# Kernel optimization log

Hardware: AMD Instinct MI355X
Metric: run time of the kernel (lower is better)

Reference implementation:

```python
import jax, jax.numpy as jnp
import numpy as np

B, N, E = 4, 25000, 1600000
NODE_DIM, EMBED = 64, 64
NUM = B * N


def setup_inputs() -> dict:
    key = jax.random.key(0)
    ks = jax.random.split(key, 12)
    p = lambda k, s: jax.random.normal(k, s, jnp.float32) * 0.05
    z = lambda s: jnp.zeros(s, jnp.float32)
    return {
        "node_feat": jax.random.normal(ks[0], (B, N, NODE_DIM), jnp.float32),
        "src": jax.random.randint(ks[1], (E,), 0, NUM),
        "dst": jax.random.randint(ks[2], (E,), 0, NUM),
        "edge_weight": jax.random.uniform(ks[3], (E,), jnp.float32),
        "h": z((NUM, EMBED)),
        "W_cz": p(ks[4], (NODE_DIM, EMBED)), "b_cz": z((EMBED,)),
        "W_cr": p(ks[5], (NODE_DIM, EMBED)), "b_cr": z((EMBED,)),
        "W_ch": p(ks[6], (NODE_DIM, EMBED)), "b_ch": z((EMBED,)),
        "W_lz": p(ks[7], (2 * EMBED, EMBED)), "b_lz": z((EMBED,)),
        "W_lr": p(ks[8], (2 * EMBED, EMBED)), "b_lr": z((EMBED,)),
        "W_lh": p(ks[9], (2 * EMBED, EMBED)), "b_lh": z((EMBED,)),
        "W_head": p(ks[10], (EMBED, 1)), "b_head": z((1,)),
    }


def gcn_conv(x, W, b, src, dst, ew):
    # PyG GCNConv: self-loops (fill=1) + symmetric normalization, then linear.
    n = x.shape[0]
    loop = jnp.arange(n)
    s = jnp.concatenate([src, loop])
    d = jnp.concatenate([dst, loop])
    w = jnp.concatenate([ew, jnp.ones((n,), x.dtype)])
    deg = jax.ops.segment_sum(w, d, num_segments=n)
    dinv = jnp.where(deg > 0, jax.lax.rsqrt(deg), 0.0)
    norm = dinv[s] * w * dinv[d]                      # [E+n]
    xw = x @ W                                        # [n, EMBED]
    out = jax.ops.segment_sum(xw[s] * norm[:, None], d, num_segments=n)
    return out + b


def tgcn_cell(x, h, src, dst, ew,
              W_cz, b_cz, W_cr, b_cr, W_ch, b_ch,
              W_lz, b_lz, W_lr, b_lr, W_lh, b_lh):
    Z = jax.nn.sigmoid(
        jnp.concatenate([gcn_conv(x, W_cz, b_cz, src, dst, ew), h], axis=1) @ W_lz + b_lz)
    R = jax.nn.sigmoid(
        jnp.concatenate([gcn_conv(x, W_cr, b_cr, src, dst, ew), h], axis=1) @ W_lr + b_lr)
    H_tilde = jnp.tanh(
        jnp.concatenate([gcn_conv(x, W_ch, b_ch, src, dst, ew), h * R], axis=1) @ W_lh + b_lh)
    return Z * h + (1.0 - Z) * H_tilde


def reference(node_feat, src, dst, edge_weight, h,
              W_cz, b_cz, W_cr, b_cr, W_ch, b_ch,
              W_lz, b_lz, W_lr, b_lr, W_lh, b_lh,
              W_head, b_head):
    Bv, Nv, _ = node_feat.shape
    x = node_feat.reshape(Bv * Nv, -1)
    h0 = tgcn_cell(x, h, src, dst, edge_weight,
                   W_cz, b_cz, W_cr, b_cr, W_ch, b_ch,
                   W_lz, b_lz, W_lr, b_lr, W_lh, b_lh)
    z = jax.nn.relu(h0)
    z = (z @ W_head + b_head).reshape(Bv, Nv, -1)
    return (z, h0)
```

## Files before the change

### kernel.cpp

```cpp
#include <hip/hip_runtime.h>
#include <hip/hip_fp16.h>
#include <stdint.h>

typedef unsigned long long u64;
typedef _Float16 half8 __attribute__((ext_vector_type(8)));
typedef float f32x4 __attribute__((ext_vector_type(4)));

#define EPB 6144
#define CAPC 5440

__device__ __forceinline__ float sigm(float x) { return 1.0f / (1.0f + __expf(-x)); }
__device__ __forceinline__ float tanhfast(float x) { return 1.0f - 2.0f / (__expf(2.0f * x) + 1.0f); }
__device__ __forceinline__ int rli(int v, int k) { return __builtin_amdgcn_readlane(v, k); }
__device__ __forceinline__ float rlf(float v, int k) {
    return __int_as_float(__builtin_amdgcn_readlane(__float_as_int(v), k));
}

__global__ void k_pre(const float* __restrict__ Wcz, const float* __restrict__ bcz,
                      const float* __restrict__ Wcr, const float* __restrict__ bcr,
                      const float* __restrict__ Wch, const float* __restrict__ bch,
                      const float* __restrict__ Wlz, const float* __restrict__ blz,
                      const float* __restrict__ Wlr, const float* __restrict__ blr,
                      const float* __restrict__ Wlh, const float* __restrict__ blh,
                      const float4* __restrict__ h4, __half* __restrict__ aggh,
                      __half* __restrict__ B1f, __half* __restrict__ B2f,
                      float* __restrict__ bias, int* __restrict__ cursor, int hq) {
    int bid = blockIdx.x;
    if (bid < 113) {
        int tid = bid * 256 + threadIdx.x;
        if (tid < 1024) cursor[tid] = 0;
        if (tid < 24576) {
            int k = tid / 192, nc = tid % 192;
            int g = nc >> 6, j = nc & 63;
            const float* Wc = (g == 0) ? Wcz : (g == 1) ? Wcr : Wch;
            const float* Wl = (g == 0) ? Wlz : (g == 1) ? Wlr : Wlh;
            float v;
            if (k < 64) {
                float acc = 0.f;
                for (int m = 0; m < 64; m++) acc += Wc[k * 64 + m] * Wl[m * 64 + j];
                v = acc;
            } else {
                v = (g < 2) ? Wl[k * 64 + j] : 0.f;
            }
            int kt = k >> 5, nt = nc >> 4;
            int lane = (((k >> 3) & 3) << 4) | (nc & 15);
            B1f[(((kt * 12 + nt) * 64 + lane) << 3) + (k & 7)] = (__half)v;
        } else if (tid < 24576 + 4096) {
            int t = tid - 24576;
            int k = t >> 6, nc = t & 63;
            float v = Wlh[(64 + k) * 64 + nc];
            int kt = k >> 5, nt = nc >> 4;
            int lane = (((k >> 3) & 3) << 4) | (nc & 15);
            B2f[(((kt * 4 + nt) * 64 + lane) << 3) + (k & 7)] = (__half)v;
        } else if (tid < 24576 + 4096 + 192) {
            int t = tid - 24576 - 4096;
            int g = t >> 6, j = t & 63;
            const float* bc = (g == 0) ? bcz : (g == 1) ? bcr : bch;
            const float* Wl = (g == 0) ? Wlz : (g == 1) ? Wlr : Wlh;
            const float* bl = (g == 0) ? blz : (g == 1) ? blr : blh;
            float acc = bl[j];
            for (int m = 0; m < 64; m++) acc += bc[m] * Wl[m * 64 + j];
            bias[t] = acc;
        }
    } else {
        int i = (bid - 113) * 256 + threadIdx.x;
        if (i < hq) {
            float4 hv = h4[i];
            int elem = i * 4;
            int node = elem >> 6, c = elem & 63;
            __half2* ho = (__half2*)(aggh + (((size_t)node) << 7) + 64 + c);
            ho[0] = __floats2half2_rn(hv.x, hv.y);
            ho[1] = __floats2half2_rn(hv.z, hv.w);
        }
    }
}

__global__ void __launch_bounds__(1024) k_bin(const int* __restrict__ src, const int* __restrict__ dst,
                                              const float* __restrict__ ew,
                                              int* __restrict__ cursor, u64* __restrict__ binned,
                                              int E, int R) {
    __shared__ u64 recs[EPB];
    __shared__ int hist[512];
    __shared__ int loff[512];
    __shared__ int curL[512];
    __shared__ int gbase[512];

    int tid = threadIdx.x;
    if (tid < 512) hist[tid] = 0;
    __syncthreads();

    int base = blockIdx.x * EPB;
    int cntE = min(EPB, E - base);

    u64 myrec[6];
    int myr[6];
#pragma unroll
    for (int j = 0; j < 6; j++) {
        int idx = tid + j * 1024;
        if (idx < cntE) {
            int e = base + idx;
            int d = dst[e], s = src[e];
            float w = ew[e];
            int r = d >> 8;
            myr[j] = r;
            myrec[j] = (u64)((unsigned)s | ((unsigned)(d & 255) << 17)) | ((u64)__float_as_uint(w) << 32);
            atomicAdd(&hist[r], 1);
        } else myr[j] = -1;
    }
    __syncthreads();

    if (tid < 64) {
        int sums[8], tot = 0;
#pragma unroll
        for (int q = 0; q < 8; q++) { sums[q] = hist[tid * 8 + q]; tot += sums[q]; }
        int scan = tot;
#pragma unroll
        for (int o = 1; o < 64; o <<= 1) {
            int v = __shfl_up(scan, o);
            if (tid >= o) scan += v;
        }
        int run = scan - tot;
#pragma unroll
        for (int q = 0; q < 8; q++) { loff[tid * 8 + q] = run; run += sums[q]; }
    }
    if (tid < 512) curL[tid] = 0;
    if (tid < R) {
        int hcnt = hist[tid];
        if (hcnt > 0) gbase[tid] = tid * CAPC + atomicAdd(&cursor[tid], hcnt);
    }
    __syncthreads();

#pragma unroll
    for (int j = 0; j < 6; j++) {
        if (myr[j] >= 0) {
            int p = atomicAdd(&curL[myr[j]], 1);
            recs[loff[myr[j]] + p] = myrec[j];
        }
    }
    __syncthreads();

    int wave = tid >> 6, lane = tid & 63;
    for (int r = wave; r < R; r += 16) {
        int len = hist[r];
        if (!len) continue;
        int gb = gbase[r], lo = loff[r];
        int capEnd = (r + 1) * CAPC;
        for (int i = lane; i < len; i += 64)
            if (gb + i < capEnd) binned[(size_t)(gb + i)] = recs[lo + i];
    }
}

__global__ void __launch_bounds__(1024) k_sort(const int* __restrict__ cursor,
                                               u64* __restrict__ binned,
                                               const float2* __restrict__ x2,
                                               float* __restrict__ dinv,
                                               __half2* __restrict__ xs2,
                                               int* __restrict__ off_g, int* __restrict__ len_g,
                                               int n) {
    __shared__ u64 srt[CAPC];
    __shared__ int hist[256];
    __shared__ int noff[256];
    __shared__ int cur[256];
    __shared__ float degw[256];

    int r = blockIdx.x, tid = threadIdx.x;
    if (tid < 256) { hist[tid] = 0; degw[tid] = 0.f; }
    __syncthreads();

    int cnt = min(cursor[r], CAPC);
    u64* B = binned + (size_t)r * CAPC;

    for (int i = tid; i < cnt; i += 1024) {
        u64 m = B[i];
        int dl = ((unsigned)m >> 17) & 255;
        atomicAdd(&hist[dl], 1);
        atomicAdd(&degw[dl], __uint_as_float((unsigned)(m >> 32)));
    }
    __syncthreads();

    if (tid < 64) {
        int s0 = hist[tid * 4], s1 = hist[tid * 4 + 1], s2 = hist[tid * 4 + 2], s3 = hist[tid * 4 + 3];
        int tot = s0 + s1 + s2 + s3;
        int scan = tot;
#pragma unroll
        for (int o = 1; o < 64; o <<= 1) {
            int v = __shfl_up(scan, o);
            if (tid >= o) scan += v;
        }
        int run = scan - tot;
        noff[tid * 4] = run; run += s0;
        noff[tid * 4 + 1] = run; run += s1;
        noff[tid * 4 + 2] = run; run += s2;
        noff[tid * 4 + 3] = run;
    }
    __syncthreads();

    if (tid < 256) {
        int node = r * 256 + tid;
        float dv = rsqrtf(1.0f + degw[tid]);
        if (node < n) {
            dinv[node] = dv;
            off_g[node] = r * CAPC + noff[tid];
            len_g[node] = hist[tid];
        }
        cur[tid] = noff[tid];
        degw[tid] = dv;
    }
    __syncthreads();

    for (int i = tid; i < cnt; i += 1024) {
        u64 m = B[i];
        int dl = ((unsigned)m >> 17) & 255;
        int p = atomicAdd(&cur[dl], 1);
        srt[p] = (u64)((unsigned)m & 0x1FFFF) | (m & 0xFFFFFFFF00000000ULL);
    }
    __syncthreads();

    for (int i = tid; i < cnt; i += 1024) B[i] = srt[i];
    int nbase = r * 256;
    for (int i = tid; i < 256 * 32; i += 1024) {
        int nl = i >> 5, cp = i & 31;
        int node = nbase + nl;
        if (node < n) {
            float2 xv = x2[((size_t)node << 5) + cp];
            float dv = degw[nl];
            xs2[((size_t)node << 5) + cp] = __floats2half2_rn(dv * xv.x, dv * xv.y);
        }
    }
}

__global__ void __launch_bounds__(256) k_gather(const int* __restrict__ off_g, const int* __restrict__ len_g,
                                                const u64* __restrict__ csr, const float* __restrict__ dinv,
                                                const __half* __restrict__ xs,
                                                __half* __restrict__ aggh, int n) {
    int lane = threadIdx.x & 63;
    int wid = __builtin_amdgcn_readfirstlane((int)(threadIdx.x >> 6));
    int d = blockIdx.x * 4 + wid;
    if (d >= n) return;
    int o0 = off_g[d], L = len_g[d];
    float dd = dinv[d];

    const uint2* __restrict__ rp = (const uint2*)(csr + (size_t)o0);

    float acc[8];
#pragma unroll
    for (int j = 0; j < 8; j++) acc[j] = 0.f;
    acc[0] = (float)xs[((size_t)d << 6) + lane];

    int k = 0;
    for (; k + 8 <= L; k += 8) {
        uint2 r[8];
#pragma unroll
        for (int j = 0; j < 8; j++) r[j] = rp[k + j];
#pragma unroll
        for (int j = 0; j < 8; j++) {
            acc[j] = fmaf(__uint_as_float(r[j].y),
                          (float)xs[((size_t)r[j].x << 6) + lane], acc[j]);
        }
    }
    for (; k < L; k++) {
        uint2 r = rp[k];
        acc[0] = fmaf(__uint_as_float(r.y),
                      (float)xs[((size_t)r.x << 6) + lane], acc[0]);
    }

    float s = ((acc[0] + acc[1]) + (acc[2] + acc[3])) + ((acc[4] + acc[5]) + (acc[6] + acc[7]));
    aggh[((size_t)d << 7) + lane] = (__half)(dd * s);
}

__global__ void __launch_bounds__(256, 2) k_node(
        const __half* __restrict__ aggh,
        const __half* __restrict__ B1f_g, const __half* __restrict__ B2f_g,
        const float* __restrict__ bias_g, const float* __restrict__ Whead,
        const float* __restrict__ bhead,
        float* __restrict__ out_head, float* __restrict__ out_h, int n) {

    __shared__ __half B1s[24576];
    __shared__ __half B2s[4096];
    __shared__ float biasS[192];
    __shared__ float whS[64];
    __shared__ __half hrb[4][16 * 72];

    int tid = threadIdx.x;
    {
        const uint4* s1 = (const uint4*)B1f_g; uint4* d1 = (uint4*)B1s;
        for (int i = tid; i < 3072; i += 256) d1[i] = s1[i];
        const uint4* s2 = (const uint4*)B2f_g; uint4* d2 = (uint4*)B2s;
        for (int i = tid; i < 512; i += 256) d2[i] = s2[i];
        if (tid < 192) biasS[tid] = bias_g[tid];
        if (tid < 64) whS[tid] = Whead[tid];
    }
    __syncthreads();

    int lane = tid & 63;
    int wave = tid >> 6;
    int quad = lane >> 4;
    int l15 = lane & 15;

    float bz4[4], br4[4], bh4[4], wh4[4];
#pragma unroll
    for (int nt = 0; nt < 4; nt++) {
        bz4[nt] = biasS[nt * 16 + l15];
        br4[nt] = biasS[64 + nt * 16 + l15];
        bh4[nt] = biasS[128 + nt * 16 + l15];
        wh4[nt] = whS[nt * 16 + l15];
    }
    float bhv = bhead[0];
    __half* myhr = &hrb[wave][0];
    const half8* B1v = (const half8*)B1s;
    const half8* B2v = (const half8*)B2s;

    int mbase = blockIdx.x * 64 + wave * 16;
    if (mbase < n) {
        const half8* arow = (const half8*)(aggh + (((size_t)(mbase + l15)) << 7) + (quad << 3));
        half8 a0 = arow[0], a1 = arow[4], a2 = arow[8], a3 = arow[12];

        f32x4 acc[12];
#pragma unroll
        for (int nt = 0; nt < 12; nt++) acc[nt] = (f32x4){0.f, 0.f, 0.f, 0.f};

#pragma unroll
        for (int nt = 0; nt < 12; nt++) {
            acc[nt] = __builtin_amdgcn_mfma_f32_16x16x32_f16(a0, B1v[(0 * 12 + nt) * 64 + lane], acc[nt], 0, 0, 0);
            acc[nt] = __builtin_amdgcn_mfma_f32_16x16x32_f16(a1, B1v[(1 * 12 + nt) * 64 + lane], acc[nt], 0, 0, 0);
            acc[nt] = __builtin_amdgcn_mfma_f32_16x16x32_f16(a2, B1v[(2 * 12 + nt) * 64 + lane], acc[nt], 0, 0, 0);
            acc[nt] = __builtin_amdgcn_mfma_f32_16x16x32_f16(a3, B1v[(3 * 12 + nt) * 64 + lane], acc[nt], 0, 0, 0);
        }

        float hv[4][4];
#pragma unroll
        for (int nt = 0; nt < 4; nt++)
#pragma unroll
            for (int r = 0; r < 4; r++)
                hv[nt][r] = (float)aggh[(((size_t)(mbase + quad * 4 + r)) << 7) + 64 + nt * 16 + l15];

        float Z[4][4];
#pragma unroll
        for (int nt = 0; nt < 4; nt++)
#pragma unroll
            for (int r = 0; r < 4; r++) {
                Z[nt][r] = sigm(acc[nt][r] + bz4[nt]);
                float R = sigm(acc[4 + nt][r] + br4[nt]);
                myhr[(quad * 4 + r) * 72 + nt * 16 + l15] = (__half)(hv[nt][r] * R);
            }
        __builtin_amdgcn_s_waitcnt(0);

        half8 a2f0 = *(const half8*)(myhr + l15 * 72 + quad * 8);
        half8 a2f1 = *(const half8*)(myhr + l15 * 72 + 32 + quad * 8);

#pragma unroll
        for (int nt = 0; nt < 4; nt++) {
            acc[8 + nt] = __builtin_amdgcn_mfma_f32_16x16x32_f16(a2f0, B2v[(0 * 4 + nt) * 64 + lane], acc[8 + nt], 0, 0, 0);
            acc[8 + nt] = __builtin_amdgcn_mfma_f32_16x16x32_f16(a2f1, B2v[(1 * 4 + nt) * 64 + lane], acc[8 + nt], 0, 0, 0);
        }

        float pr0 = 0.f, pr1 = 0.f, pr2 = 0.f, pr3 = 0.f;
#pragma unroll
        for (int nt = 0; nt < 4; nt++) {
#pragma unroll
            for (int r = 0; r < 4; r++) {
                float Ht = tanhfast(acc[8 + nt][r] + bh4[nt]);
                float z = Z[nt][r];
                float hn = z * hv[nt][r] + (1.f - z) * Ht;
                out_h[((size_t)(mbase + quad * 4 + r)) * 64 + nt * 16 + l15] = hn;
                float rv = fmaxf(hn, 0.f) * wh4[nt];
                if (r == 0) pr0 += rv; else if (r == 1) pr1 += rv; else if (r == 2) pr2 += rv; else pr3 += rv;
            }
        }
#pragma unroll
        for (int o = 1; o < 16; o <<= 1) {
            pr0 += __shfl_xor(pr0, o);
            pr1 += __shfl_xor(pr1, o);
            pr2 += __shfl_xor(pr2, o);
            pr3 += __shfl_xor(pr3, o);
        }
        if (l15 == 0) {
            out_head[mbase + quad * 4 + 0] = pr0 + bhv;
            out_head[mbase + quad * 4 + 1] = pr1 + bhv;
            out_head[mbase + quad * 4 + 2] = pr2 + bhv;
            out_head[mbase + quad * 4 + 3] = pr3 + bhv;
        }
    }
}

extern "C" void kernel_launch(void* const* d_in, const int* in_sizes, int n_in,
                              void* d_out, int out_size, void* d_ws, size_t ws_size,
                              hipStream_t stream) {
    const float* x     = (const float*)d_in[0];
    const int*   src   = (const int*)d_in[1];
    const int*   dst   = (const int*)d_in[2];
    const float* ew    = (const float*)d_in[3];
    const float* h     = (const float*)d_in[4];
    const float* Wcz   = (const float*)d_in[5];
    const float* bcz   = (const float*)d_in[6];
    const float* Wcr   = (const float*)d_in[7];
    const float* bcr   = (const float*)d_in[8];
    const float* Wch   = (const float*)d_in[9];
    const float* bch   = (const float*)d_in[10];
    const float* Wlz   = (const float*)d_in[11];
    const float* blz   = (const float*)d_in[12];
    const float* Wlr   = (const float*)d_in[13];
    const float* blr   = (const float*)d_in[14];
    const float* Wlh   = (const float*)d_in[15];
    const float* blh   = (const float*)d_in[16];
    const float* Whead = (const float*)d_in[17];
    const float* bhead = (const float*)d_in[18];

    int E = in_sizes[1];
    int n = in_sizes[4] / 64;
    int R = (n + 255) >> 8;

    __half* aggh = (__half*)d_ws;
    __half* xs   = aggh + (size_t)n * 128;
    u64*   binned = (u64*)(xs + (size_t)n * 64);
    float* dinv  = (float*)(binned + (size_t)R * CAPC);
    int*   off_g = (int*)(dinv + n);
    int*   len_g = off_g + n;
    int*   cursor = len_g + n;
    __half* B1f  = (__half*)(cursor + 1024);
    __half* B2f  = B1f + 24576;
    float* bias  = (float*)(B2f + 4096);

    float* out_head = (float*)d_out;
    float* out_h    = out_head + n;

    int hq = n * 16;
    int nbB = (E + EPB - 1) / EPB;
    int gridPre = 113 + (hq + 255) / 256;

    k_pre<<<gridPre, 256, 0, stream>>>(Wcz, bcz, Wcr, bcr, Wch, bch,
                                       Wlz, blz, Wlr, blr, Wlh, blh,
                                       (const float4*)h, aggh, B1f, B2f, bias, cursor, hq);
    k_bin<<<nbB, 1024, 0, stream>>>(src, dst, ew, cursor, binned, E, R);
    k_sort<<<R, 1024, 0, stream>>>(cursor, binned, (const float2*)x, dinv,
                                   (__half2*)xs, off_g, len_g, n);
    k_gather<<<(n + 3) / 4, 256, 0, stream>>>(off_g, len_g, binned, dinv, xs, aggh, n);
    k_node<<<(n + 63) / 64, 256, 0, stream>>>(aggh, B1f, B2f, bias, Whead, bhead,
                                              out_head, out_h, n);
}
```

Baseline: 254.9 us.

## Replace per-node CSR sort and gather with per-bin LDS atomic scatter-accumulate

Drops the per-bin counting sort that built a CSR layout (histogram, scan, shared-memory reorder and write-back) and the per-destination-node gather kernel. A per-bin kernel now has each wave broadcast edge records through readlane, load the source features, and atomically add weighted values into a 256x64 float accumulator in LDS, then add the self-loop and write the normalized result. This removes the sort pass and the off/len arrays, at the cost of heavy LDS float atomics, a 64KB LDS footprint per block that limits occupancy, and only R (~391) blocks of parallelism for the gather.

```diff
diff --git a/kernel.cpp b/kernel.cpp
--- a/kernel.cpp
+++ b/kernel.cpp
@@ -150,73 +150,36 @@
     }
 }
 
-__global__ void __launch_bounds__(1024) k_sort(const int* __restrict__ cursor,
-                                               u64* __restrict__ binned,
-                                               const float2* __restrict__ x2,
-                                               float* __restrict__ dinv,
-                                               __half2* __restrict__ xs2,
-                                               int* __restrict__ off_g, int* __restrict__ len_g,
-                                               int n) {
-    __shared__ u64 srt[CAPC];
-    __shared__ int hist[256];
-    __shared__ int noff[256];
-    __shared__ int cur[256];
+__global__ void __launch_bounds__(1024) k_deg(const int* __restrict__ cursor,
+                                              const u64* __restrict__ binned,
+                                              const float2* __restrict__ x2,
+                                              float* __restrict__ dinv,
+                                              __half2* __restrict__ xs2,
+                                              int n) {
     __shared__ float degw[256];
 
     int r = blockIdx.x, tid = threadIdx.x;
-    if (tid < 256) { hist[tid] = 0; degw[tid] = 0.f; }
+    if (tid < 256) degw[tid] = 0.f;
     __syncthreads();
 
     int cnt = min(cursor[r], CAPC);
-    u64* B = binned + (size_t)r * CAPC;
+    const u64* B = binned + (size_t)r * CAPC;
 
     for (int i = tid; i < cnt; i += 1024) {
         u64 m = B[i];
         int dl = ((unsigned)m >> 17) & 255;
-        atomicAdd(&hist[dl], 1);
         atomicAdd(&degw[dl], __uint_as_float((unsigned)(m >> 32)));
-    }
-    __syncthreads();
-
-    if (tid < 64) {
-        int s0 = hist[tid * 4], s1 = hist[tid * 4 + 1], s2 = hist[tid * 4 + 2], s3 = hist[tid * 4 + 3];
-        int tot = s0 + s1 + s2 + s3;
-        int scan = tot;
-#pragma unroll
-        for (int o = 1; o < 64; o <<= 1) {
-            int v = __shfl_up(scan, o);
-            if (tid >= o) scan += v;
-        }
-        int run = scan - tot;
-        noff[tid * 4] = run; run += s0;
-        noff[tid * 4 + 1] = run; run += s1;
-        noff[tid * 4 + 2] = run; run += s2;
-        noff[tid * 4 + 3] = run;
     }
     __syncthreads();
 
     if (tid < 256) {
         int node = r * 256 + tid;
         float dv = rsqrtf(1.0f + degw[tid]);
-        if (node < n) {
-            dinv[node] = dv;
-            off_g[node] = r * CAPC + noff[tid];
-            len_g[node] = hist[tid];
-        }
-        cur[tid] = noff[tid];
+        if (node < n) dinv[node] = dv;
         degw[tid] = dv;
     }
     __syncthreads();
 
-    for (int i = tid; i < cnt; i += 1024) {
-        u64 m = B[i];
-        int dl = ((unsigned)m >> 17) & 255;
-        int p = atomicAdd(&cur[dl], 1);
-        srt[p] = (u64)((unsigned)m & 0x1FFFF) | (m & 0xFFFFFFFF00000000ULL);
-    }
-    __syncthreads();
-
-    for (int i = tid; i < cnt; i += 1024) B[i] = srt[i];
     int nbase = r * 256;
     for (int i = tid; i < 256 * 32; i += 1024) {
         int nl = i >> 5, cp = i & 31;
@@ -229,43 +192,63 @@
     }
 }
 
-__global__ void __launch_bounds__(256) k_gather(const int* __restrict__ off_g, const int* __restrict__ len_g,
-                                                const u64* __restrict__ csr, const float* __restrict__ dinv,
-                                                const __half* __restrict__ xs,
-                                                __half* __restrict__ aggh, int n) {
-    int lane = threadIdx.x & 63;
-    int wid = __builtin_amdgcn_readfirstlane((int)(threadIdx.x >> 6));
-    int d = blockIdx.x * 4 + wid;
-    if (d >= n) return;
-    int o0 = off_g[d], L = len_g[d];
-    float dd = dinv[d];
-
-    const uint2* __restrict__ rp = (const uint2*)(csr + (size_t)o0);
-
-    float acc[8];
-#pragma unroll
-    for (int j = 0; j < 8; j++) acc[j] = 0.f;
-    acc[0] = (float)xs[((size_t)d << 6) + lane];
-
-    int k = 0;
-    for (; k + 8 <= L; k += 8) {
-        uint2 r[8];
-#pragma unroll
-        for (int j = 0; j < 8; j++) r[j] = rp[k + j];
-#pragma unroll
-        for (int j = 0; j < 8; j++) {
-            acc[j] = fmaf(__uint_as_float(r[j].y),
-                          (float)xs[((size_t)r[j].x << 6) + lane], acc[j]);
-        }
-    }
-    for (; k < L; k++) {
-        uint2 r = rp[k];
-        acc[0] = fmaf(__uint_as_float(r.y),
-                      (float)xs[((size_t)r.x << 6) + lane], acc[0]);
-    }
-
-    float s = ((acc[0] + acc[1]) + (acc[2] + acc[3])) + ((acc[4] + acc[5]) + (acc[6] + acc[7]));
-    aggh[((size_t)d << 7) + lane] = (__half)(dd * s);
+__global__ void __launch_bounds__(1024) k_gather(const int* __restrict__ cursor,
+                                                 const u64* __restrict__ binned,
+                                                 const float* __restrict__ dinv,
+                                                 const __half* __restrict__ xs,
+                                                 __half* __restrict__ aggh, int n) {
+    __shared__ float agg[256 * 64];
+
+    int tid = threadIdx.x;
+    int lane = tid & 63;
+    int wave = __builtin_amdgcn_readfirstlane((int)(tid >> 6));
+
+    {
+        f32x4* a4 = (f32x4*)agg;
+        for (int i = tid; i < 256 * 16; i += 1024) a4[i] = (f32x4){0.f, 0.f, 0.f, 0.f};
+    }
+    __syncthreads();
+
+    int r = blockIdx.x;
+    int cnt = min(cursor[r], CAPC);
+    const u64* B = binned + (size_t)r * CAPC;
+
+    for (int base = wave * 64; base < cnt; base += 1024) {
+        int c = min(64, cnt - base);
+        u64 m = (lane < c) ? B[base + lane] : 0;
+        int lo_l = (int)(unsigned)m;
+        float w_l = __uint_as_float((unsigned)(m >> 32));
+
+        int k = 0;
+        for (; k + 8 <= c; k += 8) {
+            int lo[8]; float ww[8], xr[8];
+#pragma unroll
+            for (int j = 0; j < 8; j++) { lo[j] = rli(lo_l, k + j); ww[j] = rlf(w_l, k + j); }
+#pragma unroll
+            for (int j = 0; j < 8; j++)
+                xr[j] = (float)xs[((size_t)(lo[j] & 0x1FFFF) << 6) + lane];
+#pragma unroll
+            for (int j = 0; j < 8; j++)
+                atomicAdd(&agg[(((lo[j] >> 17) & 255) << 6) + lane], ww[j] * xr[j]);
+        }
+        for (; k < c; k++) {
+            int lo = rli(lo_l, k);
+            float ww = rlf(w_l, k);
+            float xr = (float)xs[((size_t)(lo & 0x1FFFF) << 6) + lane];
+            atomicAdd(&agg[(((lo >> 17) & 255) << 6) + lane], ww * xr);
+        }
+    }
+    __syncthreads();
+
+    int nbase = r * 256;
+    for (int i = tid; i < 256 * 64; i += 1024) {
+        int dl = i >> 6, cc = i & 63;
+        int node = nbase + dl;
+        if (node < n) {
+            float s = agg[i] + (float)xs[((size_t)node << 6) + cc];
+            aggh[((size_t)node << 7) + cc] = (__half)(dinv[node] * s);
+        }
+    }
 }
 
 __global__ void __launch_bounds__(256, 2) k_node(
@@ -414,9 +397,7 @@
     __half* xs   = aggh + (size_t)n * 128;
     u64*   binned = (u64*)(xs + (size_t)n * 64);
     float* dinv  = (float*)(binned + (size_t)R * CAPC);
-    int*   off_g = (int*)(dinv + n);
-    int*   len_g = off_g + n;
-    int*   cursor = len_g + n;
+    int*   cursor = (int*)(dinv + n);
     __half* B1f  = (__half*)(cursor + 1024);
     __half* B2f  = B1f + 24576;
     float* bias  = (float*)(B2f + 4096);
@@ -432,9 +413,9 @@
                                        Wlz, blz, Wlr, blr, Wlh, blh,
                                        (const float4*)h, aggh, B1f, B2f, bias, cursor, hq);
     k_bin<<<nbB, 1024, 0, stream>>>(src, dst, ew, cursor, binned, E, R);
-    k_sort<<<R, 1024, 0, stream>>>(cursor, binned, (const float2*)x, dinv,
-                                   (__half2*)xs, off_g, len_g, n);
-    k_gather<<<(n + 3) / 4, 256, 0, stream>>>(off_g, len_g, binned, dinv, xs, aggh, n);
+    k_deg<<<R, 1024, 0, stream>>>(cursor, binned, (const float2*)x, dinv,
+                                  (__half2*)xs, n);
+    k_gather<<<R, 1024, 0, stream>>>(cursor, binned, dinv, xs, aggh, n);
     k_node<<<(n + 63) / 64, 256, 0, stream>>>(aggh, B1f, B2f, bias, Whead, bhead,
                                               out_head, out_h, n);
 }
```

Result: slower. 881.0 us (+245.7%).
